# Kernel tuning notes

Hardware: AMD Instinct MI355X
Metric: run time of the kernel (lower is better)

## Reference

```python
import jax, jax.numpy as jnp
import numpy as np

N = 100      # num sensors/nodes
C = 32       # channels (hard-coded in module)
H = 512      # hidden_size (hard-coded)
T = 64       # window_size (lags)
B = 16       # batch
E = 2000     # edges = N * topk
HORIZON = 10


def _arma(x, ei, ew, W, V, b, n):
    # ARMAConv, num_stacks=1, num_layers=1, GELU act, dropout off (eval)
    h = x @ W                                    # (n, C)
    row, col = ei[0], ei[1]
    deg = jax.ops.segment_sum(ew, col, num_segments=n)
    dinv = jnp.where(deg > 0, 1.0 / jnp.sqrt(jnp.maximum(deg, 1e-12)), 0.0)
    norm = dinv[row] * ew * dinv[col]            # gcn_norm, no self loops
    agg = jax.ops.segment_sum(norm[:, None] * h[row], col, num_segments=n)
    return jax.nn.gelu(agg + x @ V + b, approximate=False)


def _lstm_step(h, c, xt, Wih, Whh, bih, bhh):
    g = xt @ Wih.T + h @ Whh.T + bih + bhh
    i, f, gg, o = jnp.split(g, 4, axis=-1)       # torch gate order i,f,g,o
    c = jax.nn.sigmoid(f) * c + jax.nn.sigmoid(i) * jnp.tanh(gg)
    h = jax.nn.sigmoid(o) * jnp.tanh(c)
    return h, c


def _lstm_layer(xs, Wih, Whh, bih, bhh):
    # xs: (T, B, in) -> outputs (T, B, H), final h
    Bn = xs.shape[1]
    init = (jnp.zeros((Bn, H), xs.dtype), jnp.zeros((Bn, H), xs.dtype))
    def step(carry, xt):
        hc = _lstm_step(carry[0], carry[1], xt, Wih, Whh, bih, bhh)
        return hc, hc[0]
    (hT, cT), hs = jax.lax.scan(step, init, xs)
    return hs, hT


def setup_inputs() -> dict:
    key = jax.random.key(0)
    ks = jax.random.split(key, 20)
    s = 0.05
    def nrm(k, shape):
        return jax.random.normal(k, shape, jnp.float32) * s
    ei = jax.random.randint(ks[1], (2, E), 0, N)
    ei = ei.at[0, 0].set(N - 1).at[1, 0].set(N - 1)  # ensure max node id present
    z = lambda *sh: jnp.zeros(sh, jnp.float32)
    return {
        "window": jax.random.normal(ks[0], (B * N, T), jnp.float32),
        "edge_index": ei,
        "edge_attr": jax.random.uniform(ks[2], (E,), jnp.float32),
        "W_embed": nrm(ks[3], (N, C)),
        "tg_w": nrm(ks[4], (1, C)), "tg_v": nrm(ks[5], (1, C)), "tg_b": z(C),
        "gnn_w": nrm(ks[6], (1, C)), "gnn_v": nrm(ks[7], (1, C)), "gnn_b": z(C),
        "lstm_Wih0": nrm(ks[8], (4 * H, N * C)), "lstm_Whh0": nrm(ks[9], (4 * H, H)),
        "lstm_bih0": z(4 * H), "lstm_bhh0": z(4 * H),
        "lstm_Wih1": nrm(ks[10], (4 * H, H)), "lstm_Whh1": nrm(ks[11], (4 * H, H)),
        "lstm_bih1": z(4 * H), "lstm_bhh1": z(4 * H),
        "c1_Wih": nrm(ks[12], (4 * H, N * C)), "c1_Whh": nrm(ks[13], (4 * H, H)),
        "c1_bih": z(4 * H), "c1_bhh": z(4 * H),
        "c2_Wih": nrm(ks[14], (4 * H, H)), "c2_Whh": nrm(ks[15], (4 * H, H)),
        "c2_bih": z(4 * H), "c2_bhh": z(4 * H),
        "Wp": nrm(ks[16], (N, H)), "bp": z(N),
    }


def _forward(edge_index, window, edge_attr, W_embed, tg_w, tg_v, tg_b,
             gnn_w, gnn_v, gnn_b,
             lstm_Wih0, lstm_Whh0, lstm_bih0, lstm_bhh0,
             lstm_Wih1, lstm_Whh1, lstm_bih1, lstm_bhh1,
             c1_Wih, c1_Whh, c1_bih, c1_bhh,
             c2_Wih, c2_Whh, c2_bih, c2_bhh, Wp, bp):
    BN = B * N
    # batch edges over B (offset b*N), exactly as the torch offset arithmetic
    bi = (edge_index[:, None, :] + (jnp.arange(B) * N)[None, :, None]).reshape(2, B * E)
    battr = jnp.tile(edge_attr, B)
    # temporal batching inside TGConv: offsets t*(B*N) on node-major flat x
    ti = (bi[:, None, :] + (jnp.arange(T) * BN)[None, :, None]).reshape(2, T * B * E)
    tattr = jnp.tile(battr, T)
    x = _arma(window.reshape(BN * T, 1), ti, tattr, tg_w, tg_v, tg_b, BN * T)  # (BN*T, C)
    x = x.reshape(B, N, T, C).transpose(0, 2, 1, 3) + W_embed                 # (B,T,N,C)
    x = x.reshape(B, T, N * C).transpose(1, 0, 2)                             # (T,B,NC)
    hs0, h1f = _lstm_layer(x, lstm_Wih0, lstm_Whh0, lstm_bih0, lstm_bhh0)
    hs1, h2f = _lstm_layer(hs0, lstm_Wih1, lstm_Whh1, lstm_bih1, lstm_bhh1)
    # original assigns (h_n, h_n): cell states seeded from hidden states
    def step(carry, _):
        h1, c1, h2, c2 = carry
        pred = h2 @ Wp.T + bp                      # (B, N)
        g = _arma(pred.reshape(BN, 1), bi, battr, gnn_w, gnn_v, gnn_b, BN)
        xin = (g.reshape(B, N, C) + W_embed).reshape(B, N * C)
        h1n, c1n = _lstm_step(h1, c1, xin, c1_Wih, c1_Whh, c1_bih, c1_bhh)
        h2n, c2n = _lstm_step(h2, c2, h1n, c2_Wih, c2_Whh, c2_bih, c2_bhh)
        return (h1n, c1n, h2n, c2n), pred.reshape(-1)
    _, preds = jax.lax.scan(step, (h1f, h1f, h2f, h2f), None, length=HORIZON)
    return preds.T                                  # (B*N, HORIZON)


def reference(window, edge_index, edge_attr, W_embed, tg_w, tg_v, tg_b,
              gnn_w, gnn_v, gnn_b,
              lstm_Wih0, lstm_Whh0, lstm_bih0, lstm_bhh0,
              lstm_Wih1, lstm_Whh1, lstm_bih1, lstm_bhh1,
              c1_Wih, c1_Whh, c1_bih, c1_bhh,
              c2_Wih, c2_Whh, c2_bih, c2_bhh, Wp, bp):
    return _forward(edge_index, window, edge_attr, W_embed, tg_w, tg_v, tg_b,
                    gnn_w, gnn_v, gnn_b,
                    lstm_Wih0, lstm_Whh0, lstm_bih0, lstm_bhh0,
                    lstm_Wih1, lstm_Whh1, lstm_bih1, lstm_bhh1,
                    c1_Wih, c1_Whh, c1_bih, c1_bhh,
                    c2_Wih, c2_Whh, c2_bih, c2_bhh, Wp, bp)
```

## Files before the change

kernel.cpp:

```cpp
#include <hip/hip_runtime.h>
#include <math.h>

#define HZN 10
#define NBLK 256

__device__ __forceinline__ float sigm(float x) { return 1.f / (1.f + expf(-x)); }
__device__ __forceinline__ float gelu_f(float x) { return 0.5f * x * (1.f + erff(x * 0.70710678118654752f)); }

__device__ __forceinline__ float cLd(const float* p) {
  return __hip_atomic_load(p, __ATOMIC_RELAXED, __HIP_MEMORY_SCOPE_AGENT);
}
__device__ __forceinline__ void cSt(float* p, float v) {
  __hip_atomic_store(p, v, __ATOMIC_RELAXED, __HIP_MEMORY_SCOPE_AGENT);
}
__device__ __forceinline__ unsigned cLdU(const unsigned* p) {
  return __hip_atomic_load(p, __ATOMIC_RELAXED, __HIP_MEMORY_SCOPE_AGENT);
}
__device__ __forceinline__ void cStU(unsigned* p, unsigned v) {
  __hip_atomic_store(p, v, __ATOMIC_RELAXED, __HIP_MEMORY_SCOPE_AGENT);
}
__device__ __forceinline__ void vfence() {
  asm volatile("s_waitcnt vmcnt(0)" ::: "memory");
}

__device__ __forceinline__ float blo(unsigned u) { return __uint_as_float(u << 16); }
__device__ __forceinline__ float bhi(unsigned u) { return __uint_as_float(u & 0xffff0000u); }
__device__ __forceinline__ unsigned bfu(float x) {
  unsigned u = __float_as_uint(x);
  return (u + 0x7fffu + ((u >> 16) & 1u)) >> 16;
}
__device__ __forceinline__ unsigned packbf(float a, float b) {
  return bfu(a) | (bfu(b) << 16);
}

__device__ __forceinline__ void gbar(unsigned* flags, unsigned* gen, int bid, int tid, unsigned& bgen) {
  ++bgen;
  vfence();
  __syncthreads();
  if (bid == 0) {
    if (tid > 0 && tid < NBLK) {
      while (cLdU(&flags[tid]) < bgen) __builtin_amdgcn_s_sleep(1);
    }
    __syncthreads();
    if (tid == 0) cStU(gen, bgen);
  } else {
    if (tid == 0) {
      cStU(&flags[bid], bgen);
      while (cLdU(gen) < bgen) __builtin_amdgcn_s_sleep(1);
    }
    __syncthreads();
  }
}

__global__ void setup_kernel(const int* __restrict__ ei, const float* __restrict__ ew,
                             int* __restrict__ cptr, int* __restrict__ csrc, float* __restrict__ cnorm) {
  __shared__ float deg[100];
  __shared__ float dinv[100];
  __shared__ int cnt[100];
  __shared__ int pos[100];
  __shared__ int ptr[101];
  const int t = threadIdx.x;
  if (t < 100) { deg[t] = 0.f; cnt[t] = 0; }
  __syncthreads();
  for (int e = t; e < 2000; e += 256) {
    int c = ei[2000 + e];
    atomicAdd(&deg[c], ew[e]);
    atomicAdd(&cnt[c], 1);
  }
  __syncthreads();
  if (t < 100) dinv[t] = (deg[t] > 0.f) ? 1.f / sqrtf(fmaxf(deg[t], 1e-12f)) : 0.f;
  if (t == 0) {
    ptr[0] = 0;
    for (int n = 0; n < 100; ++n) ptr[n + 1] = ptr[n] + cnt[n];
  }
  __syncthreads();
  if (t < 100) pos[t] = ptr[t];
  if (t < 101) cptr[t] = ptr[t];
  __syncthreads();
  for (int e = t; e < 2000; e += 256) {
    int r = ei[e], c = ei[2000 + e];
    int p = atomicAdd(&pos[c], 1);
    csrc[p] = r;
    cnorm[p] = dinv[r] * ew[e] * dinv[c];
  }
}

__global__ void pack_rows(const float* __restrict__ A, const float* __restrict__ B,
                          int Ka, int Kb, int rows, unsigned* __restrict__ out) {
  int K2 = (Ka + Kb) >> 1;
  long idx = (long)blockIdx.x * 256 + threadIdx.x;
  if (idx >= (long)rows * K2) return;
  int row = idx / K2, q = idx - (long)row * K2;
  int j0 = 2 * q;
  float a = (j0 < Ka) ? A[(long)row * Ka + j0] : B[(long)row * Kb + (j0 - Ka)];
  float b = (j0 + 1 < Ka) ? A[(long)row * Ka + j0 + 1] : B[(long)row * Kb + (j0 + 1 - Ka)];
  out[idx] = packbf(a, b);
}

__global__ void xs_kernel(const float* __restrict__ win,
                          const int* __restrict__ cptr, const int* __restrict__ csrc,
                          const float* __restrict__ cnorm,
                          const float* __restrict__ tgw, const float* __restrict__ tgv,
                          const float* __restrict__ tgb, const float* __restrict__ Wemb,
                          float* __restrict__ XS) {
  const int g = blockIdx.x * 256 + threadIdx.x;
  if (g >= 102400) return;
  const int n2 = g % 100;
  const int base = g - n2;
  float s = 0.f;
  const int p0 = cptr[n2], p1 = cptr[n2 + 1];
  for (int p = p0; p < p1; ++p) s += cnorm[p] * win[base + csrc[p]];
  const float x = win[g];
  const int t = g % 64;
  const int bb = g / 6400;
  const int n = (g / 64) % 100;
  float* dst = XS + (size_t)(t * 16 + bb) * 3200 + n * 32;
  for (int c = 0; c < 32; ++c) {
    float v = s * tgw[c] + x * tgv[c] + tgb[c];
    dst[c] = gelu_f(v) + Wemb[n * 32 + c];
  }
}

__global__ __launch_bounds__(256) void g0_gemm(const float* __restrict__ XS, const float* __restrict__ W,
                                               const float* __restrict__ b1, const float* __restrict__ b2,
                                               float* __restrict__ G0) {
  __shared__ float As[16][68];
  __shared__ float Bs[16][68];
  const int tid = threadIdx.x;
  const int m0 = blockIdx.y * 64, n0 = blockIdx.x * 64;
  const int tx = tid & 15, ty = tid >> 4;
  const int lr = tid >> 2, lk = (tid & 3) * 4;
  float acc[4][4] = {};
  for (int k0 = 0; k0 < 3200; k0 += 16) {
    float4 av = *(const float4*)&XS[(size_t)(m0 + lr) * 3200 + k0 + lk];
    float4 bv = *(const float4*)&W[(size_t)(n0 + lr) * 3200 + k0 + lk];
    As[lk + 0][lr] = av.x; As[lk + 1][lr] = av.y; As[lk + 2][lr] = av.z; As[lk + 3][lr] = av.w;
    Bs[lk + 0][lr] = bv.x; Bs[lk + 1][lr] = bv.y; Bs[lk + 2][lr] = bv.z; Bs[lk + 3][lr] = bv.w;
    __syncthreads();
#pragma unroll
    for (int kk = 0; kk < 16; ++kk) {
      float4 a = *(const float4*)&As[kk][ty * 4];
      float4 b = *(const float4*)&Bs[kk][tx * 4];
      acc[0][0] += a.x * b.x; acc[0][1] += a.x * b.y; acc[0][2] += a.x * b.z; acc[0][3] += a.x * b.w;
      acc[1][0] += a.y * b.x; acc[1][1] += a.y * b.y; acc[1][2] += a.y * b.z; acc[1][3] += a.y * b.w;
      acc[2][0] += a.z * b.x; acc[2][1] += a.z * b.y; acc[2][2] += a.z * b.z; acc[2][3] += a.z * b.w;
      acc[3][0] += a.w * b.x; acc[3][1] += a.w * b.y; acc[3][2] += a.w * b.z; acc[3][3] += a.w * b.w;
    }
    __syncthreads();
  }
#pragma unroll
  for (int i = 0; i < 4; ++i) {
    const int m = m0 + ty * 4 + i;
#pragma unroll
    for (int j = 0; j < 4; ++j) {
      const int nn = n0 + tx * 4 + j;
      G0[(size_t)m * 2048 + nn] = acc[i][j] + b1[nn] + b2[nn];
    }
  }
}

struct ScanArgs {
  const float* G0;
  const unsigned* W0p;
  const unsigned* W1p;
  const float* bih1; const float* bhh1;
  float* hs0;
  float* h1ex;
  unsigned* F0;
  unsigned* F1;
};

__global__ __launch_bounds__(512, 1) void scan_kernel(ScanArgs A) {
  __shared__ float hl[1024];
  const int tid = threadIdx.x;
  const int bid = blockIdx.x;
  const int hf = tid & 1;
  const int u = tid >> 3;
  const int g = (tid >> 1) & 3;

  if (bid < 128) {
    const int b = bid >> 3, j = bid & 7;
    const int wrow = g * 512 + j * 64 + u;
    const uint4* wp = (const uint4*)A.W0p + (size_t)wrow * 64 + hf * 32;
    const float4* hl4 = (const float4*)hl + hf * 64;
    float c0r = 0.f;
    for (int t = 0; t < 64; ++t) {
      if (t > 0) {
        if (tid < 8) {
          while (cLdU(&A.F0[b * 8 + tid]) < (unsigned)t) {}
        }
        __syncthreads();
        hl[tid & 511] = cLd(&A.hs0[((size_t)(t - 1) * 16 + b) * 512 + (tid & 511)]);
        __syncthreads();
      }
      float acc = 0.f;
      if (t > 0) {
#pragma unroll 8
        for (int i = 0; i < 32; ++i) {
          uint4 w = wp[i];
          float4 ha = hl4[2 * i], hb2 = hl4[2 * i + 1];
          acc += blo(w.x) * ha.x + bhi(w.x) * ha.y + blo(w.y) * ha.z + bhi(w.y) * ha.w;
          acc += blo(w.z) * hb2.x + bhi(w.z) * hb2.y + blo(w.w) * hb2.z + bhi(w.w) * hb2.w;
        }
      }
      acc += __shfl_xor(acc, 1);
      float gF = __shfl_xor(acc, 2);
      float gG = __shfl_xor(acc, 4);
      float gO = __shfl_xor(acc, 6);
      if ((tid & 7) == 0) {
        const float* g0r = A.G0 + ((size_t)t * 16 + b) * 2048 + j * 64;
        float gi = acc + g0r[u];
        float gf = gF + g0r[512 + u];
        float gg = gG + g0r[1024 + u];
        float go = gO + g0r[1536 + u];
        c0r = sigm(gf) * c0r + sigm(gi) * tanhf(gg);
        float hn = sigm(go) * tanhf(c0r);
        cSt(&A.hs0[((size_t)t * 16 + b) * 512 + j * 64 + u], hn);
      }
      vfence();
      __syncthreads();
      if (tid == 0) cStU(&A.F0[b * 8 + j], t + 1);
    }
  } else {
    const int b = (bid - 128) >> 3, j = bid & 7;
    const int wrow = g * 512 + j * 64 + u;
    const uint4* wp = (const uint4*)A.W1p + (size_t)wrow * 128 + hf * 64;
    const float4* hl4 = (const float4*)hl + hf * 128;
    float c1s = 0.f;
    float bI = 0.f, bF = 0.f, bG = 0.f, bO = 0.f;
    if ((tid & 7) == 0) {
      int uu = j * 64 + u;
      bI = A.bih1[uu] + A.bhh1[uu];
      bF = A.bih1[512 + uu] + A.bhh1[512 + uu];
      bG = A.bih1[1024 + uu] + A.bhh1[1024 + uu];
      bO = A.bih1[1536 + uu] + A.bhh1[1536 + uu];
    }
    for (int t = 0; t < 64; ++t) {
      if (tid < 8) {
        while (cLdU(&A.F0[b * 8 + tid]) < (unsigned)(t + 1)) {}
      } else if (tid < 16) {
        if (t > 0) { while (cLdU(&A.F1[b * 8 + (tid - 8)]) < (unsigned)t) {} }
      }
      __syncthreads();
      hl[tid] = cLd(&A.hs0[((size_t)t * 16 + b) * 512 + tid]);
      hl[512 + tid] = (t > 0) ? cLd(&A.h1ex[(((t - 1) & 1) * 16 + b) * 512 + tid]) : 0.f;
      __syncthreads();
      float acc = 0.f;
#pragma unroll 8
      for (int i = 0; i < 64; ++i) {
        uint4 w = wp[i];
        float4 ha = hl4[2 * i], hb2 = hl4[2 * i + 1];
        acc += blo(w.x) * ha.x + bhi(w.x) * ha.y + blo(w.y) * ha.z + bhi(w.y) * ha.w;
        acc += blo(w.z) * hb2.x + bhi(w.z) * hb2.y + blo(w.w) * hb2.z + bhi(w.w) * hb2.w;
      }
      acc += __shfl_xor(acc, 1);
      float gF = __shfl_xor(acc, 2);
      float gG = __shfl_xor(acc, 4);
      float gO = __shfl_xor(acc, 6);
      if ((tid & 7) == 0) {
        float gi = acc + bI, gf = gF + bF, gg = gG + bG, go = gO + bO;
        c1s = sigm(gf) * c1s + sigm(gi) * tanhf(gg);
        float hn = sigm(go) * tanhf(c1s);
        cSt(&A.h1ex[((t & 1) * 16 + b) * 512 + j * 64 + u], hn);
      }
      vfence();
      __syncthreads();
      if (tid == 0) cStU(&A.F1[b * 8 + j], t + 1);
    }
  }
}

struct DecArgs {
  const unsigned* c1Wih2;
  const unsigned* c1Whh2;
  const float* c1bih; const float* c1bhh;
  const unsigned* c2W2;
  const float* c2bih; const float* c2bhh;
  const float* Wp; const float* bp;
  const float* gw; const float* gv; const float* gb;
  const float* Wemb;
  const int* cptr; const int* csrc; const float* cnorm;
  const float* hs0;
  const float* h1ex;
  float* xinE; float* xinO;
  unsigned* h1pk;
  unsigned* h2pk;
  float* h2f;
  unsigned* bflags; unsigned* gen;
  float* out;
};

#define DX_E 0
#define DX_O 12800
#define DH1E 25600
#define DH1O 27648
#define DGATE 29696

__global__ __launch_bounds__(512, 1) void dec_kernel(DecArgs A) {
  extern __shared__ float lds[];
  const int tid = threadIdx.x;
  const int bid = blockIdx.x;
  unsigned bgen = 0;

  const int u0 = bid * 2;
  float* xeven = lds + DX_E;
  float* xodd = lds + DX_O;
  float* h1e = lds + DH1E;
  float* h1o = lds + DH1O;
  float* gatel = lds + DGATE;

  const int nstart = (bid * 1600) >> 8;
  const int nend = ((bid + 1) * 1600) >> 8;
  const int ncnt = nend - nstart;
  const int nb0 = nstart / 100;

  float c1reg[2];
  float c2reg = 0.f;
  if (tid < 16) {
#pragma unroll
    for (int p = 0; p < 2; ++p) {
      int bl = tid >> 1, du = tid & 1;
      c1reg[p] = cLd(&A.hs0[((size_t)63 * 16 + p * 8 + bl) * 512 + u0 + du]);
    }
  }
  if (tid < 32) {
    int bl = tid >> 1, du = tid & 1;
    c2reg = cLd(&A.h1ex[(1 * 16 + bl) * 512 + u0 + du]);
  }

  for (int hz = 0; hz < HZN; ++hz) {
    const int cur = hz & 1, nxt = cur ^ 1;

    {
      float* h2l = lds;
      float* predd = lds + 1024;
      float* dnrm = lds + 1536;
      float* s2l = lds + 2048;
      float* pl = lds + 2064;
      int* doffs = (int*)(lds + 2080);
      int* dcnts = (int*)(lds + 2096);
      int* dsrc = (int*)(lds + 2112);
      int* dli = (int*)(lds + 2624);
      int* dtot = (int*)(lds + 3136);

      for (int k = 0; k < 2; ++k) {
        int i = k * 512 + tid;
        int bb = i >> 9, uu = i & 511;
        int bidx = nb0 + bb; if (bidx > 15) bidx = 15;
        float v = (hz == 0) ? cLd(&A.h1ex[(16 + bidx) * 512 + uu])
                            : cLd(&A.h2f[((size_t)cur * 16 + bidx) * 512 + uu]);
        h2l[i] = v;
      }
      if (tid < ncnt) {
        int gg = nstart + tid, n = gg % 100;
        dcnts[tid] = A.cptr[n + 1] - A.cptr[n] + 1;
      }
      __syncthreads();
      if (tid == 0) {
        int D = 0;
        for (int q = 0; q < ncnt; ++q) { doffs[q] = D; D += dcnts[q]; }
        *dtot = D;
      }
      __syncthreads();
      if (tid < ncnt) {
        int q = tid, gg = nstart + q, n = gg % 100;
        int o = doffs[q];
        dsrc[o] = n; dli[o] = q; dnrm[o] = 0.f;
        int p0 = A.cptr[n], p1 = A.cptr[n + 1];
        for (int p = p0; p < p1; ++p) {
          ++o;
          dsrc[o] = A.csrc[p]; dli[o] = q; dnrm[o] = A.cnorm[p];
        }
      }
      __syncthreads();
      const int D = *dtot;
      const int dslot = tid >> 4, ln = tid & 15;
      for (int base = 0; base < D; base += 32) {
        int dd = base + dslot;
        if (dd < D) {
          int q = dli[dd];
          int gg = nstart + q;
          int bloc = gg / 100 - nb0;
          int src = dsrc[dd];
          const float* hr = h2l + bloc * 512;
          const float* wr = A.Wp + src * 512;
          float a = 0.f;
#pragma unroll
          for (int kk = 0; kk < 32; ++kk) { int jx = kk * 16 + ln; a += hr[jx] * wr[jx]; }
          a += __shfl_xor(a, 1); a += __shfl_xor(a, 2); a += __shfl_xor(a, 4); a += __shfl_xor(a, 8);
          if (ln == 0) predd[dd] = a + A.bp[src];
        }
      }
      __syncthreads();
      if (tid < ncnt) {
        int q = tid;
        int o = doffs[q], c2n = dcnts[q];
        float s2 = 0.f;
        for (int p = 1; p < c2n; ++p) s2 += dnrm[o + p] * predd[o + p];
        s2l[q] = s2;
        float pv = predd[o];
        pl[q] = pv;
        A.out[(size_t)(nstart + q) * HZN + hz] = pv;
      }
      __syncthreads();
      if (tid < ncnt * 32) {
        int q = tid >> 5, c = tid & 31;
        int gg = nstart + q, b = gg / 100, n = gg % 100;
        float v = s2l[q] * A.gw[c] + pl[q] * A.gv[c] + A.gb[c];
        float xv = gelu_f(v) + A.Wemb[n * 32 + c];
        int pi = n * 16 + (c >> 1);
        if (c & 1) cSt(&A.xinO[(size_t)b * 1600 + pi], xv);
        else       cSt(&A.xinE[(size_t)b * 1600 + pi], xv);
      }
    }
    gbar(A.bflags, A.gen, bid, tid, bgen);

#pragma unroll
    for (int p = 0; p < 2; ++p) {
      const int B0 = p * 8;
      for (int k = 0; k < 50; ++k) {
        int idx = k * 512 + tid;
        int half = idx / 12800;
        int r2 = idx - half * 12800;
        int bb = r2 / 1600, q = r2 - bb * 1600;
        float v = half ? cLd(&A.xinO[(size_t)(B0 + bb) * 1600 + q])
                       : cLd(&A.xinE[(size_t)(B0 + bb) * 1600 + q]);
        if (half) xodd[r2] = v; else xeven[r2] = v;
      }
      for (int k = 0; k < 4; ++k) {
        int i = k * 512 + tid;
        int bb = i >> 8, pp = i & 255;
        float x0, x1;
        if (hz == 0) {
          x0 = cLd(&A.hs0[((size_t)63 * 16 + B0 + bb) * 512 + 2 * pp]);
          x1 = cLd(&A.hs0[((size_t)63 * 16 + B0 + bb) * 512 + 2 * pp + 1]);
        } else {
          unsigned pk = cLdU(&A.h1pk[((size_t)cur * 16 + B0 + bb) * 256 + pp]);
          x0 = blo(pk); x1 = bhi(pk);
        }
        h1e[bb * 256 + pp] = x0;
        h1o[bb * 256 + pp] = x1;
      }
      __syncthreads();
      {
        float acc[8] = {};
        const int r_ = tid >> 6, ks = tid & 63;
        const int wrow = (r_ >> 1) * 512 + u0 + (r_ & 1);
        for (int jj = 0; jj < 25; ++jj) {
          int pi = jj * 64 + ks;
          unsigned w = A.c1Wih2[(size_t)wrow * 1600 + pi];
          float wl = blo(w), wh = bhi(w);
#pragma unroll
          for (int bb = 0; bb < 8; ++bb) {
            acc[bb] += wl * xeven[bb * 1600 + pi] + wh * xodd[bb * 1600 + pi];
          }
        }
        for (int jj = 0; jj < 4; ++jj) {
          int pi = jj * 64 + ks;
          unsigned w = A.c1Whh2[wrow * 256 + pi];
          float wl = blo(w), wh = bhi(w);
#pragma unroll
          for (int bb = 0; bb < 8; ++bb) {
            acc[bb] += wl * h1e[bb * 256 + pi] + wh * h1o[bb * 256 + pi];
          }
        }
#pragma unroll
        for (int bb = 0; bb < 8; ++bb) {
          float v = acc[bb];
          v += __shfl_xor(v, 32); v += __shfl_xor(v, 16); v += __shfl_xor(v, 8);
          v += __shfl_xor(v, 4); v += __shfl_xor(v, 2); v += __shfl_xor(v, 1);
          acc[bb] = v;
        }
        if (ks == 0) {
#pragma unroll
          for (int bb = 0; bb < 8; ++bb) gatel[r_ * 8 + bb] = acc[bb];
        }
      }
      __syncthreads();
      if (tid < 16) {
        int bl = tid >> 1, du = tid & 1;
        int uu = u0 + du;
        float gi = gatel[(0 + du) * 8 + bl] + A.c1bih[uu] + A.c1bhh[uu];
        float gf = gatel[(2 + du) * 8 + bl] + A.c1bih[512 + uu] + A.c1bhh[512 + uu];
        float gg = gatel[(4 + du) * 8 + bl] + A.c1bih[1024 + uu] + A.c1bhh[1024 + uu];
        float go = gatel[(6 + du) * 8 + bl] + A.c1bih[1536 + uu] + A.c1bhh[1536 + uu];
        float cn = sigm(gf) * c1reg[p] + sigm(gi) * tanhf(gg);
        float hn = sigm(go) * tanhf(cn);
        c1reg[p] = cn;
        float ho = __shfl(hn, tid ^ 1);
        if (du == 0) cStU(&A.h1pk[((size_t)nxt * 16 + B0 + bl) * 256 + bid], packbf(hn, ho));
      }
      __syncthreads();
    }
    gbar(A.bflags, A.gen, bid, tid, bgen);

    {
      unsigned* h1b = (unsigned*)lds;
      unsigned* h2b = (unsigned*)lds + 4096;
      for (int k = 0; k < 8; ++k) {
        int i = k * 512 + tid;
        int bb = i >> 8, pp = i & 255;
        h1b[i] = cLdU(&A.h1pk[((size_t)nxt * 16 + bb) * 256 + pp]);
        unsigned v2;
        if (hz == 0) {
          float x0 = cLd(&A.h1ex[(16 + bb) * 512 + 2 * pp]);
          float x1 = cLd(&A.h1ex[(16 + bb) * 512 + 2 * pp + 1]);
          v2 = packbf(x0, x1);
        } else {
          v2 = cLdU(&A.h2pk[((size_t)cur * 16 + bb) * 256 + pp]);
        }
        h2b[i] = v2;
      }
      __syncthreads();
      float acc[16] = {};
      const int r_ = tid >> 6, ks = tid & 63;
      const int wrow = (r_ >> 1) * 512 + u0 + (r_ & 1);
      for (int jj = 0; jj < 8; ++jj) {
        int pi = jj * 64 + ks;
        unsigned w = A.c2W2[wrow * 512 + pi];
        float wl = blo(w), wh = bhi(w);
        const unsigned* hsrc = (pi < 256) ? h1b : (h2b - 256);
#pragma unroll
        for (int bb = 0; bb < 16; ++bb) {
          unsigned hv = hsrc[bb * 256 + pi];
          acc[bb] += wl * blo(hv) + wh * bhi(hv);
        }
      }
#pragma unroll
      for (int bb = 0; bb < 16; ++bb) {
        float v = acc[bb];
        v += __shfl_xor(v, 32); v += __shfl_xor(v, 16); v += __shfl_xor(v, 8);
        v += __shfl_xor(v, 4); v += __shfl_xor(v, 2); v += __shfl_xor(v, 1);
        acc[bb] = v;
      }
      if (ks == 0) {
#pragma unroll
        for (int bb = 0; bb < 16; ++bb) gatel[r_ * 16 + bb] = acc[bb];
      }
      __syncthreads();
      if (tid < 32) {
        int bl = tid >> 1, du = tid & 1;
        int uu = u0 + du;
        float gi = gatel[(0 + du) * 16 + bl] + A.c2bih[uu] + A.c2bhh[uu];
        float gf = gatel[(2 + du) * 16 + bl] + A.c2bih[512 + uu] + A.c2bhh[512 + uu];
        float gg = gatel[(4 + du) * 16 + bl] + A.c2bih[1024 + uu] + A.c2bhh[1024 + uu];
        float go = gatel[(6 + du) * 16 + bl] + A.c2bih[1536 + uu] + A.c2bhh[1536 + uu];
        float cn = sigm(gf) * c2reg + sigm(gi) * tanhf(gg);
        float hn = sigm(go) * tanhf(cn);
        c2reg = cn;
        cSt(&A.h2f[((size_t)nxt * 16 + bl) * 512 + uu], hn);
        float ho = __shfl(hn, tid ^ 1);
        if (du == 0) cStU(&A.h2pk[((size_t)nxt * 16 + bl) * 256 + bid], packbf(hn, ho));
      }
      __syncthreads();
    }
    gbar(A.bflags, A.gen, bid, tid, bgen);
  }
}

extern "C" void kernel_launch(void* const* d_in, const int* in_sizes, int n_in,
                              void* d_out, int out_size, void* d_ws, size_t ws_size,
                              hipStream_t stream) {
  (void)in_sizes; (void)n_in; (void)out_size; (void)ws_size;
  const float* window = (const float*)d_in[0];
  const int* ei = (const int*)d_in[1];
  const float* ew = (const float*)d_in[2];
  const float* Wemb = (const float*)d_in[3];
  const float* tgw = (const float*)d_in[4];
  const float* tgv = (const float*)d_in[5];
  const float* tgb = (const float*)d_in[6];
  const float* gw = (const float*)d_in[7];
  const float* gv = (const float*)d_in[8];
  const float* gb = (const float*)d_in[9];
  const float* Wih0 = (const float*)d_in[10];
  const float* Whh0 = (const float*)d_in[11];
  const float* bih0 = (const float*)d_in[12];
  const float* bhh0 = (const float*)d_in[13];
  const float* Wih1 = (const float*)d_in[14];
  const float* Whh1 = (const float*)d_in[15];
  const float* bih1 = (const float*)d_in[16];
  const float* bhh1 = (const float*)d_in[17];
  const float* c1Wih = (const float*)d_in[18];
  const float* c1Whh = (const float*)d_in[19];
  const float* c1bih = (const float*)d_in[20];
  const float* c1bhh = (const float*)d_in[21];
  const float* c2Wih = (const float*)d_in[22];
  const float* c2Whh = (const float*)d_in[23];
  const float* c2bih = (const float*)d_in[24];
  const float* c2bhh = (const float*)d_in[25];
  const float* Wp = (const float*)d_in[26];
  const float* bp = (const float*)d_in[27];

  char* w = (char*)d_ws;
  size_t off = 0;
  auto alloc = [&](size_t bytes) { void* p = w + off; off = (off + bytes + 255) & ~(size_t)255; return p; };
  int* cptr = (int*)alloc(101 * 4);
  int* csrc = (int*)alloc(2000 * 4);
  float* cnorm = (float*)alloc(2000 * 4);
  float* XS = (float*)alloc((size_t)1024 * 3200 * 4);
  float* G0 = (float*)alloc((size_t)1024 * 2048 * 4);
  unsigned* W0p = (unsigned*)alloc((size_t)2048 * 256 * 4);
  unsigned* W1p = (unsigned*)alloc((size_t)2048 * 512 * 4);
  unsigned* c1Wih2 = (unsigned*)alloc((size_t)2048 * 1600 * 4);
  unsigned* c1Whh2 = (unsigned*)alloc((size_t)2048 * 256 * 4);
  unsigned* c2W2 = (unsigned*)alloc((size_t)2048 * 512 * 4);
  float* hs0 = (float*)alloc((size_t)64 * 16 * 512 * 4);
  float* h1ex = (float*)alloc((size_t)2 * 16 * 512 * 4);
  float* xinE = (float*)alloc((size_t)16 * 1600 * 4);
  float* xinO = (float*)alloc((size_t)16 * 1600 * 4);
  unsigned* h1pk = (unsigned*)alloc((size_t)2 * 16 * 256 * 4);
  unsigned* h2pk = (unsigned*)alloc((size_t)2 * 16 * 256 * 4);
  float* h2f = (float*)alloc((size_t)2 * 16 * 512 * 4);
  unsigned* flagzone = (unsigned*)alloc((128 + 128 + 256 + 16) * 4);
  unsigned* F0 = flagzone;
  unsigned* F1 = flagzone + 128;
  unsigned* bflags = flagzone + 256;
  unsigned* gen = flagzone + 512;

  hipMemsetAsync(flagzone, 0, (128 + 128 + 256 + 16) * 4, stream);

  setup_kernel<<<1, 256, 0, stream>>>(ei, ew, cptr, csrc, cnorm);
  pack_rows<<<(2048 * 256 + 255) / 256, 256, 0, stream>>>(Whh0, nullptr, 512, 0, 2048, W0p);
  pack_rows<<<(2048 * 512 + 255) / 256, 256, 0, stream>>>(Wih1, Whh1, 512, 512, 2048, W1p);
  pack_rows<<<(int)(((size_t)2048 * 1600 + 255) / 256), 256, 0, stream>>>(c1Wih, nullptr, 3200, 0, 2048, c1Wih2);
  pack_rows<<<(2048 * 256 + 255) / 256, 256, 0, stream>>>(c1Whh, nullptr, 512, 0, 2048, c1Whh2);
  pack_rows<<<(2048 * 512 + 255) / 256, 256, 0, stream>>>(c2Wih, c2Whh, 512, 512, 2048, c2W2);
  xs_kernel<<<400, 256, 0, stream>>>(window, cptr, csrc, cnorm, tgw, tgv, tgb, Wemb, XS);
  g0_gemm<<<dim3(32, 16), 256, 0, stream>>>(XS, Wih0, bih0, bhh0, G0);

  ScanArgs S;
  S.G0 = G0; S.W0p = W0p; S.W1p = W1p;
  S.bih1 = bih1; S.bhh1 = bhh1;
  S.hs0 = hs0; S.h1ex = h1ex;
  S.F0 = F0; S.F1 = F1;
  void* sp[] = { &S };
  hipLaunchCooperativeKernel(scan_kernel, dim3(256), dim3(512), sp, 0, stream);

  DecArgs D;
  D.c1Wih2 = c1Wih2; D.c1Whh2 = c1Whh2; D.c1bih = c1bih; D.c1bhh = c1bhh;
  D.c2W2 = c2W2; D.c2bih = c2bih; D.c2bhh = c2bhh;
  D.Wp = Wp; D.bp = bp; D.gw = gw; D.gv = gv; D.gb = gb; D.Wemb = Wemb;
  D.cptr = cptr; D.csrc = csrc; D.cnorm = cnorm;
  D.hs0 = hs0; D.h1ex = h1ex;
  D.xinE = xinE; D.xinO = xinO;
  D.h1pk = h1pk; D.h2pk = h2pk; D.h2f = h2f;
  D.bflags = bflags; D.gen = gen;
  D.out = (float*)d_out;
  void* dp[] = { &D };
  hipLaunchCooperativeKernel(dec_kernel, dim3(256), dim3(512), dp, 29952 * 4, stream);
}
```

Baseline: 2.266 ms.

## Replace per-step flag handshakes with step tags packed into hidden-state words

The low 8 mantissa bits of each published hidden-state float now carry a step tag. Consumers spin directly on the data word they need instead of waiting on per-block flag counters. This removes the vmcnt fence, the extra __syncthreads and the separate flag store from every recurrent step of both LSTM layers, shortening the cross-block latency chain. In exchange, hidden states lose 8 bits of mantissa precision, the state buffers must be zeroed before launch, and every thread polls global memory with short sleeps.

Measured after the change: 2.186 ms. 3.5% less time.

```diff
diff --git a/kernel.cpp b/kernel.cpp
--- a/kernel.cpp
+++ b/kernel.cpp
@@ -164,10 +164,8 @@
   const unsigned* W0p;
   const unsigned* W1p;
   const float* bih1; const float* bhh1;
-  float* hs0;
-  float* h1ex;
-  unsigned* F0;
-  unsigned* F1;
+  unsigned* hs0u;
+  unsigned* h1exu;
 };
 
 __global__ __launch_bounds__(512, 1) void scan_kernel(ScanArgs A) {
@@ -186,11 +184,12 @@
     float c0r = 0.f;
     for (int t = 0; t < 64; ++t) {
       if (t > 0) {
-        if (tid < 8) {
-          while (cLdU(&A.F0[b * 8 + tid]) < (unsigned)t) {}
-        }
+        const unsigned tag = (unsigned)t & 0xFFu;
+        const unsigned* p = &A.hs0u[(size_t)(t - 1) * 8192 + b * 512 + (tid & 511)];
+        unsigned uu = cLdU(p);
+        while ((uu & 0xFFu) != tag) { __builtin_amdgcn_s_sleep(2); uu = cLdU(p); }
         __syncthreads();
-        hl[tid & 511] = cLd(&A.hs0[((size_t)(t - 1) * 16 + b) * 512 + (tid & 511)]);
+        hl[tid & 511] = __uint_as_float(uu & 0xFFFFFF00u);
         __syncthreads();
       }
       float acc = 0.f;
@@ -215,11 +214,9 @@
         float go = gO + g0r[1536 + u];
         c0r = sigm(gf) * c0r + sigm(gi) * tanhf(gg);
         float hn = sigm(go) * tanhf(c0r);
-        cSt(&A.hs0[((size_t)t * 16 + b) * 512 + j * 64 + u], hn);
-      }
-      vfence();
-      __syncthreads();
-      if (tid == 0) cStU(&A.F0[b * 8 + j], t + 1);
+        unsigned hw = (__float_as_uint(hn) & 0xFFFFFF00u) | ((unsigned)(t + 1) & 0xFFu);
+        cStU(&A.hs0u[(size_t)t * 8192 + b * 512 + j * 64 + u], hw);
+      }
     }
   } else {
     const int b = (bid - 128) >> 3, j = bid & 7;
@@ -236,14 +233,20 @@
       bO = A.bih1[1536 + uu] + A.bhh1[1536 + uu];
     }
     for (int t = 0; t < 64; ++t) {
-      if (tid < 8) {
-        while (cLdU(&A.F0[b * 8 + tid]) < (unsigned)(t + 1)) {}
-      } else if (tid < 16) {
-        if (t > 0) { while (cLdU(&A.F1[b * 8 + (tid - 8)]) < (unsigned)t) {} }
-      }
-      __syncthreads();
-      hl[tid] = cLd(&A.hs0[((size_t)t * 16 + b) * 512 + tid]);
-      hl[512 + tid] = (t > 0) ? cLd(&A.h1ex[(((t - 1) & 1) * 16 + b) * 512 + tid]) : 0.f;
+      const unsigned tagA = (unsigned)(t + 1) & 0xFFu;
+      const unsigned* pa = &A.hs0u[(size_t)t * 8192 + b * 512 + tid];
+      unsigned ua = cLdU(pa);
+      while ((ua & 0xFFu) != tagA) { __builtin_amdgcn_s_sleep(2); ua = cLdU(pa); }
+      unsigned ub = 0u;
+      if (t > 0) {
+        const unsigned tagB = (unsigned)t & 0xFFu;
+        const unsigned* pb = &A.h1exu[(size_t)((t - 1) & 1) * 8192 + b * 512 + tid];
+        ub = cLdU(pb);
+        while ((ub & 0xFFu) != tagB) { __builtin_amdgcn_s_sleep(2); ub = cLdU(pb); }
+      }
+      __syncthreads();
+      hl[tid] = __uint_as_float(ua & 0xFFFFFF00u);
+      hl[512 + tid] = (t > 0) ? __uint_as_float(ub & 0xFFFFFF00u) : 0.f;
       __syncthreads();
       float acc = 0.f;
 #pragma unroll 8
@@ -261,11 +264,9 @@
         float gi = acc + bI, gf = gF + bF, gg = gG + bG, go = gO + bO;
         c1s = sigm(gf) * c1s + sigm(gi) * tanhf(gg);
         float hn = sigm(go) * tanhf(c1s);
-        cSt(&A.h1ex[((t & 1) * 16 + b) * 512 + j * 64 + u], hn);
-      }
-      vfence();
-      __syncthreads();
-      if (tid == 0) cStU(&A.F1[b * 8 + j], t + 1);
+        unsigned hw = (__float_as_uint(hn) & 0xFFFFFF00u) | ((unsigned)(t + 1) & 0xFFu);
+        cStU(&A.h1exu[(size_t)(t & 1) * 8192 + b * 512 + j * 64 + u], hw);
+      }
     }
   }
 }
@@ -612,12 +613,12 @@
   unsigned* h2pk = (unsigned*)alloc((size_t)2 * 16 * 256 * 4);
   float* h2f = (float*)alloc((size_t)2 * 16 * 512 * 4);
   unsigned* flagzone = (unsigned*)alloc((128 + 128 + 256 + 16) * 4);
-  unsigned* F0 = flagzone;
-  unsigned* F1 = flagzone + 128;
   unsigned* bflags = flagzone + 256;
   unsigned* gen = flagzone + 512;
 
   hipMemsetAsync(flagzone, 0, (128 + 128 + 256 + 16) * 4, stream);
+  hipMemsetAsync(hs0, 0, (size_t)64 * 16 * 512 * 4, stream);
+  hipMemsetAsync(h1ex, 0, (size_t)2 * 16 * 512 * 4, stream);
 
   setup_kernel<<<1, 256, 0, stream>>>(ei, ew, cptr, csrc, cnorm);
   pack_rows<<<(2048 * 256 + 255) / 256, 256, 0, stream>>>(Whh0, nullptr, 512, 0, 2048, W0p);
@@ -631,8 +632,7 @@
   ScanArgs S;
   S.G0 = G0; S.W0p = W0p; S.W1p = W1p;
   S.bih1 = bih1; S.bhh1 = bhh1;
-  S.hs0 = hs0; S.h1ex = h1ex;
-  S.F0 = F0; S.F1 = F1;
+  S.hs0u = (unsigned*)hs0; S.h1exu = (unsigned*)h1ex;
   void* sp[] = { &S };
   hipLaunchCooperativeKernel(scan_kernel, dim3(256), dim3(512), sp, 0, stream);
 
```
